# Optimization experiments

Hardware: AMD Instinct MI355X
Metric: run time of the kernel (lower is better)

The kernel has to match this reference:

```python
import jax, jax.numpy as jnp
from jax import lax
import numpy as np

B, C, H, W = 32, 256, 56, 56
K = 3
EPS = 1e-5


def setup_inputs() -> dict:
    key = jax.random.key(0)
    k1, k2, k3, k4 = jax.random.split(key, 4)
    x = jax.random.normal(k1, (B, C, H, W), dtype=jnp.float32)
    # xavier_normal init for conv weight [C_out, C_in, K, K]
    fan_in = C * K * K
    fan_out = C * K * K
    std = float(np.sqrt(2.0 / (fan_in + fan_out)))
    w = jax.random.normal(k2, (C, C, K, K), dtype=jnp.float32) * std
    gamma = jnp.ones((C,), dtype=jnp.float32)
    beta = jnp.zeros((C,), dtype=jnp.float32)
    return {"x": x, "w": w, "gamma": gamma, "beta": beta}


def reference(x, w, gamma, beta):
    # --- Binarize (bi_act_method=0, bi_w_scale=1) ---
    bx = jnp.sign(x)                                   # activation sign
    wc = jnp.clip(w, -1.0, 1.0)                        # fp_weight.data.clamp_(-1,1)
    mean_val = jnp.mean(jnp.abs(wc))
    bw = jnp.sign(wc) * mean_val                       # sign(w) * mean(|w|)
    # --- float conv2d, stride 1, padding 1 ---
    out = lax.conv_general_dilated(
        bx, bw, window_strides=(1, 1), padding=[(1, 1), (1, 1)],
        dimension_numbers=("NCHW", "OIHW", "NCHW"))
    # --- identity shortcut (stride=1, C_in==C_out) ---
    out = out + x
    # --- BatchNorm2d (training-mode batch stats, affine) ---
    mean = jnp.mean(out, axis=(0, 2, 3), keepdims=True)
    var = jnp.var(out, axis=(0, 2, 3), keepdims=True)
    out = (out - mean) * lax.rsqrt(var + EPS)
    out = out * gamma[None, :, None, None] + beta[None, :, None, None]
    # --- ReLU ---
    return jax.nn.relu(out)
```

## Files before the change

### kernel.cpp

```cpp
#include <hip/hip_runtime.h>
#include <cstdint>
#include <cstring>

#define Bn   32
#define Cn   256
#define Hn   56
#define Wn   56
#define HWn  (Hn*Wn)
#define NTOT (Bn*Cn*HWn)
#define WELEMS (Cn*Cn*9)
#define EPSv 1e-5f

#define F_WABS  0
#define F_SUM   64
#define F_SQ    320
#define F_SCALE 576
#define F_SHIFT 832
#define STATS_BYTES 4352
#define WB_OFF_BYTES  8192
#define XB_OFF_BYTES  131072

__global__ void pack_w_kernel(const float* __restrict__ w,
                              float* __restrict__ wsf,
                              uint32_t* __restrict__ wb) {
    int u = blockIdx.x * 256 + threadIdx.x;
    float sabs = 0.0f;
    {
        int co = u / 72;
        int r  = u % 72;
        int t  = r >> 3;
        int wd = r & 7;
        uint32_t bits = 0;
        const float* wp = w + (size_t)co * 2304 + (size_t)(wd * 32) * 9 + t;
        #pragma unroll
        for (int j = 0; j < 32; j++) {
            float wv = wp[(size_t)j * 9];
            sabs += fminf(fabsf(wv), 1.0f);
            bits |= (__float_as_uint(wv) >> 31) << j;
        }
        wb[u] = bits;
    }
    #pragma unroll
    for (int off = 32; off; off >>= 1) sabs += __shfl_down(sabs, off);
    __shared__ float sh[4];
    if ((threadIdx.x & 63) == 0) sh[threadIdx.x >> 6] = sabs;
    __syncthreads();
    if (threadIdx.x == 0)
        atomicAdd(&wsf[F_WABS], sh[0] + sh[1] + sh[2] + sh[3]);
}

__global__ void pack_x_kernel(const float* __restrict__ x,
                              uint32_t* __restrict__ xb) {
    int v = blockIdx.x * 256 + threadIdx.x;
    int b = v / HWn;
    int p = v % HWn;
    const float* xp = x + (size_t)b * Cn * HWn + p;
    uint32_t r[8];
    #pragma unroll
    for (int wd = 0; wd < 8; wd++) {
        uint32_t bits = 0;
        #pragma unroll
        for (int j = 0; j < 32; j++) {
            bits |= (__float_as_uint(xp[(size_t)(wd * 32 + j) * HWn]) >> 31) << j;
        }
        r[wd] = bits;
    }
    uint4* d = (uint4*)xb + (size_t)v * 2;
    d[0] = make_uint4(r[0], r[1], r[2], r[3]);
    d[1] = make_uint4(r[4], r[5], r[6], r[7]);
}

__global__ __launch_bounds__(256) void conv_kernel(
    const uint32_t* __restrict__ xb, const uint32_t* __restrict__ wb,
    const float* __restrict__ x, const float* __restrict__ wsf,
    float* __restrict__ out) {
    const int by  = blockIdx.x;
    const int cog = blockIdx.y;
    const int b   = blockIdx.z;
    const int tid = threadIdx.x;
    const int ty = tid >> 6, tx = tid & 63;
    const int y = by * 4 + ty;
    const bool active = tx < Wn;
    const int lx = tx < 55 ? tx : 55;

    const float mean_val = wsf[F_WABS] * (1.0f / (float)WELEMS);

    uint32_t nw[3][24];
    #pragma unroll
    for (int dh = 0; dh < 3; dh++) {
        int yy = y + dh - 1;
        int yc = yy < 0 ? 0 : (yy > 55 ? 55 : yy);
        const uint4* p = (const uint4*)xb + ((size_t)(b * HWn + yc * Wn + lx) * 2) - 2;
        uint4 q0 = p[0], q1 = p[1], q2 = p[2], q3 = p[3], q4 = p[4], q5 = p[5];
        nw[dh][0]=q0.x;  nw[dh][1]=q0.y;  nw[dh][2]=q0.z;  nw[dh][3]=q0.w;
        nw[dh][4]=q1.x;  nw[dh][5]=q1.y;  nw[dh][6]=q1.z;  nw[dh][7]=q1.w;
        nw[dh][8]=q2.x;  nw[dh][9]=q2.y;  nw[dh][10]=q2.z; nw[dh][11]=q2.w;
        nw[dh][12]=q3.x; nw[dh][13]=q3.y; nw[dh][14]=q3.z; nw[dh][15]=q3.w;
        nw[dh][16]=q4.x; nw[dh][17]=q4.y; nw[dh][18]=q4.z; nw[dh][19]=q4.w;
        nw[dh][20]=q5.x; nw[dh][21]=q5.y; nw[dh][22]=q5.z; nw[dh][23]=q5.w;
    }

    const int co0 = cog * 4;
    int pop[4] = {0, 0, 0, 0};
    int nv = 0;
    #pragma unroll
    for (int dh = 0; dh < 3; dh++) {
        bool rok = (unsigned)(y + dh - 1) < 56u;
        #pragma unroll
        for (int dw = 0; dw < 3; dw++) {
            bool ok = rok && ((unsigned)(tx + dw - 1) < 56u);
            if (ok) {
                nv++;
                #pragma unroll
                for (int cs = 0; cs < 4; cs++) {
                    const uint32_t* wp = wb + (size_t)(co0 + cs) * 72 + (dh * 3 + dw) * 8;
                    int pc = 0;
                    #pragma unroll
                    for (int wd = 0; wd < 8; wd++)
                        pc += __popc(nw[dh][dw * 8 + wd] ^ wp[wd]);
                    pop[cs] += pc;
                }
            }
        }
    }

    if (active) {
        #pragma unroll
        for (int cs = 0; cs < 4; cs++) {
            int c = co0 + cs;
            size_t idx = (size_t)(b * Cn + c) * HWn + y * Wn + tx;
            float dot = (float)(256 * nv - 2 * pop[cs]);
            out[idx] = mean_val * dot + x[idx];
        }
    }
}

__global__ void stats_kernel(const float* __restrict__ out,
                             float* __restrict__ wsf) {
    int plane = blockIdx.x;
    const float4* p = (const float4*)(out + (size_t)plane * HWn);
    float s = 0.0f, q = 0.0f;
    for (int i = threadIdx.x; i < HWn / 4; i += 256) {
        float4 v = p[i];
        s += v.x + v.y + v.z + v.w;
        q += v.x * v.x + v.y * v.y + v.z * v.z + v.w * v.w;
    }
    #pragma unroll
    for (int off = 32; off; off >>= 1) {
        s += __shfl_down(s, off);
        q += __shfl_down(q, off);
    }
    __shared__ float ss[4], sq[4];
    if ((threadIdx.x & 63) == 0) { ss[threadIdx.x >> 6] = s; sq[threadIdx.x >> 6] = q; }
    __syncthreads();
    if (threadIdx.x == 0) {
        int c = plane & 255;
        atomicAdd(&wsf[F_SUM + c], ss[0] + ss[1] + ss[2] + ss[3]);
        atomicAdd(&wsf[F_SQ  + c], sq[0] + sq[1] + sq[2] + sq[3]);
    }
}

__global__ void bnfinal_kernel(const float* __restrict__ g,
                               const float* __restrict__ bt,
                               float* __restrict__ wsf) {
    int c = threadIdx.x;
    const float n = (float)(Bn * HWn);
    float mean = wsf[F_SUM + c] / n;
    float var  = wsf[F_SQ + c] / n - mean * mean;
    float sc = g[c] * rsqrtf(var + EPSv);
    wsf[F_SCALE + c] = sc;
    wsf[F_SHIFT + c] = bt[c] - mean * sc;
}

__global__ void epilogue_kernel(float* __restrict__ out,
                                const float* __restrict__ wsf) {
    int i = blockIdx.x * 256 + threadIdx.x;
    float4* o4 = (float4*)out;
    float4 v = o4[i];
    int c = (i / (HWn / 4)) & 255;
    float sc = wsf[F_SCALE + c];
    float sh = wsf[F_SHIFT + c];
    v.x = fmaxf(v.x * sc + sh, 0.0f);
    v.y = fmaxf(v.y * sc + sh, 0.0f);
    v.z = fmaxf(v.z * sc + sh, 0.0f);
    v.w = fmaxf(v.w * sc + sh, 0.0f);
    o4[i] = v;
}

extern "C" void kernel_launch(void* const* d_in, const int* in_sizes, int n_in,
                              void* d_out, int out_size, void* d_ws, size_t ws_size,
                              hipStream_t stream) {
    const float* x     = (const float*)d_in[0];
    const float* w     = (const float*)d_in[1];
    const float* gamma = (const float*)d_in[2];
    const float* beta  = (const float*)d_in[3];
    float* out = (float*)d_out;

    float*    wsf = (float*)d_ws;
    uint32_t* wb  = (uint32_t*)((char*)d_ws + WB_OFF_BYTES);
    uint32_t* xb  = (uint32_t*)((char*)d_ws + XB_OFF_BYTES);

    hipMemsetAsync(d_ws, 0, STATS_BYTES, stream);
    pack_w_kernel<<<dim3(72), dim3(256), 0, stream>>>(w, wsf, wb);
    pack_x_kernel<<<dim3(392), dim3(256), 0, stream>>>(x, xb);
    conv_kernel<<<dim3(14, 64, 32), dim3(256), 0, stream>>>(xb, wb, x, wsf, out);
    stats_kernel<<<dim3(Bn * Cn), dim3(256), 0, stream>>>(out, wsf);
    bnfinal_kernel<<<dim3(1), dim3(256), 0, stream>>>(gamma, beta, wsf);
    epilogue_kernel<<<dim3(NTOT / 4 / 256), dim3(256), 0, stream>>>(out, wsf);
}
```

Measured before the change: 357.1 us.

## Use zero-padded bit-packed input with border correction table; widen output channels per thread

Packs sign bits into a zero-padded 58x58 layout so the conv inner loop has no boundary branches. Padding is corrected per output pixel with a precomputed per-channel table of weight popcount sums for each of nine border classes. Each thread now computes 8 output channels over a flat pixel index instead of 4, and the BN finalize step is folded into a per-plane epilogue. The cost is an extra memset of the padded buffer, an extra small kernel, and more registers per thread.

```diff
diff --git a/kernel.cpp b/kernel.cpp
--- a/kernel.cpp
+++ b/kernel.cpp
@@ -1,6 +1,5 @@
 #include <hip/hip_runtime.h>
 #include <cstdint>
-#include <cstring>
 
 #define Bn   32
 #define Cn   256
@@ -11,14 +10,17 @@
 #define WELEMS (Cn*Cn*9)
 #define EPSv 1e-5f
 
+#define PR   58
+#define PPB  (PR*PR)
+
 #define F_WABS  0
 #define F_SUM   64
 #define F_SQ    320
-#define F_SCALE 576
-#define F_SHIFT 832
-#define STATS_BYTES 4352
-#define WB_OFF_BYTES  8192
-#define XB_OFF_BYTES  131072
+#define STATS_BYTES 4096
+#define CLS_OFF_BYTES 4096
+#define WB_OFF_BYTES  16384
+#define XB_OFF_BYTES  98304
+#define XB_BYTES (Bn*PPB*8*4)
 
 __global__ void pack_w_kernel(const float* __restrict__ w,
                               float* __restrict__ wsf,
@@ -49,11 +51,40 @@
         atomicAdd(&wsf[F_WABS], sh[0] + sh[1] + sh[2] + sh[3]);
 }
 
+__global__ void wtable_kernel(const uint32_t* __restrict__ wb,
+                              int* __restrict__ clst) {
+    int co = threadIdx.x;
+    int wp[9];
+    #pragma unroll
+    for (int t = 0; t < 9; t++) {
+        int s = 0;
+        #pragma unroll
+        for (int wd = 0; wd < 8; wd++) s += __popc(wb[(co * 9 + t) * 8 + wd]);
+        wp[t] = 256 - 2 * s;
+    }
+    int T = wp[0] + wp[1] + wp[2];
+    int Bm = wp[6] + wp[7] + wp[8];
+    int L = wp[0] + wp[3] + wp[6];
+    int R = wp[2] + wp[5] + wp[8];
+    int* o = clst + co * 9;
+    o[0] = 0;
+    o[1] = L;
+    o[2] = R;
+    o[3] = T;
+    o[4] = T + L - wp[0];
+    o[5] = T + R - wp[2];
+    o[6] = Bm;
+    o[7] = Bm + L - wp[6];
+    o[8] = Bm + R - wp[8];
+}
+
 __global__ void pack_x_kernel(const float* __restrict__ x,
                               uint32_t* __restrict__ xb) {
     int v = blockIdx.x * 256 + threadIdx.x;
     int b = v / HWn;
-    int p = v % HWn;
+    int p = v - b * HWn;
+    int y = p / Wn;
+    int xq = p - y * Wn;
     const float* xp = x + (size_t)b * Cn * HWn + p;
     uint32_t r[8];
     #pragma unroll
@@ -65,73 +96,63 @@
         }
         r[wd] = bits;
     }
-    uint4* d = (uint4*)xb + (size_t)v * 2;
+    size_t dst = (size_t)b * PPB + (size_t)(y + 1) * PR + (xq + 1);
+    uint4* d = (uint4*)xb + dst * 2;
     d[0] = make_uint4(r[0], r[1], r[2], r[3]);
     d[1] = make_uint4(r[4], r[5], r[6], r[7]);
 }
 
 __global__ __launch_bounds__(256) void conv_kernel(
     const uint32_t* __restrict__ xb, const uint32_t* __restrict__ wb,
+    const int* __restrict__ clst,
     const float* __restrict__ x, const float* __restrict__ wsf,
     float* __restrict__ out) {
-    const int by  = blockIdx.x;
-    const int cog = blockIdx.y;
-    const int b   = blockIdx.z;
-    const int tid = threadIdx.x;
-    const int ty = tid >> 6, tx = tid & 63;
-    const int y = by * 4 + ty;
-    const bool active = tx < Wn;
-    const int lx = tx < 55 ? tx : 55;
+    int v = blockIdx.x * 256 + threadIdx.x;
+    int b = v / HWn;
+    int p = v - b * HWn;
+    int y = p / Wn;
+    int xq = p - y * Wn;
+    int co0 = blockIdx.y * 8;
 
     const float mean_val = wsf[F_WABS] * (1.0f / (float)WELEMS);
 
-    uint32_t nw[3][24];
+    const uint4* base = (const uint4*)xb + ((size_t)b * PPB + (size_t)y * PR + xq) * 2;
+
+    int acc[8] = {0, 0, 0, 0, 0, 0, 0, 0};
     #pragma unroll
     for (int dh = 0; dh < 3; dh++) {
-        int yy = y + dh - 1;
-        int yc = yy < 0 ? 0 : (yy > 55 ? 55 : yy);
-        const uint4* p = (const uint4*)xb + ((size_t)(b * HWn + yc * Wn + lx) * 2) - 2;
-        uint4 q0 = p[0], q1 = p[1], q2 = p[2], q3 = p[3], q4 = p[4], q5 = p[5];
-        nw[dh][0]=q0.x;  nw[dh][1]=q0.y;  nw[dh][2]=q0.z;  nw[dh][3]=q0.w;
-        nw[dh][4]=q1.x;  nw[dh][5]=q1.y;  nw[dh][6]=q1.z;  nw[dh][7]=q1.w;
-        nw[dh][8]=q2.x;  nw[dh][9]=q2.y;  nw[dh][10]=q2.z; nw[dh][11]=q2.w;
-        nw[dh][12]=q3.x; nw[dh][13]=q3.y; nw[dh][14]=q3.z; nw[dh][15]=q3.w;
-        nw[dh][16]=q4.x; nw[dh][17]=q4.y; nw[dh][18]=q4.z; nw[dh][19]=q4.w;
-        nw[dh][20]=q5.x; nw[dh][21]=q5.y; nw[dh][22]=q5.z; nw[dh][23]=q5.w;
-    }
-
-    const int co0 = cog * 4;
-    int pop[4] = {0, 0, 0, 0};
-    int nv = 0;
-    #pragma unroll
-    for (int dh = 0; dh < 3; dh++) {
-        bool rok = (unsigned)(y + dh - 1) < 56u;
+        uint32_t nw[24];
+        const uint4* rp = base + dh * (PR * 2);
+        #pragma unroll
+        for (int q = 0; q < 6; q++) {
+            uint4 t = rp[q];
+            nw[q * 4 + 0] = t.x; nw[q * 4 + 1] = t.y;
+            nw[q * 4 + 2] = t.z; nw[q * 4 + 3] = t.w;
+        }
         #pragma unroll
         for (int dw = 0; dw < 3; dw++) {
-            bool ok = rok && ((unsigned)(tx + dw - 1) < 56u);
-            if (ok) {
-                nv++;
+            #pragma unroll
+            for (int cs = 0; cs < 8; cs++) {
+                const uint32_t* wp = wb + ((size_t)(co0 + cs) * 9 + (dh * 3 + dw)) * 8;
+                int pc = acc[cs];
                 #pragma unroll
-                for (int cs = 0; cs < 4; cs++) {
-                    const uint32_t* wp = wb + (size_t)(co0 + cs) * 72 + (dh * 3 + dw) * 8;
-                    int pc = 0;
-                    #pragma unroll
-                    for (int wd = 0; wd < 8; wd++)
-                        pc += __popc(nw[dh][dw * 8 + wd] ^ wp[wd]);
-                    pop[cs] += pc;
-                }
+                for (int wd = 0; wd < 8; wd++)
+                    pc += __popc(nw[dw * 8 + wd] ^ wp[wd]);
+                acc[cs] = pc;
             }
         }
     }
 
-    if (active) {
-        #pragma unroll
-        for (int cs = 0; cs < 4; cs++) {
-            int c = co0 + cs;
-            size_t idx = (size_t)(b * Cn + c) * HWn + y * Wn + tx;
-            float dot = (float)(256 * nv - 2 * pop[cs]);
-            out[idx] = mean_val * dot + x[idx];
-        }
+    int yp = (y == 0) ? 1 : ((y == 55) ? 2 : 0);
+    int xp = (xq == 0) ? 1 : ((xq == 55) ? 2 : 0);
+    int cls = yp * 3 + xp;
+
+    #pragma unroll
+    for (int cs = 0; cs < 8; cs++) {
+        int corr = clst[(co0 + cs) * 9 + cls];
+        size_t idx = ((size_t)b * Cn + (co0 + cs)) * HWn + p;
+        float dot = (float)(2304 - 2 * acc[cs] - corr);
+        out[idx] = fmaf(mean_val, dot, x[idx]);
     }
 }
 
@@ -160,31 +181,26 @@
     }
 }
 
-__global__ void bnfinal_kernel(const float* __restrict__ g,
-                               const float* __restrict__ bt,
-                               float* __restrict__ wsf) {
-    int c = threadIdx.x;
+__global__ void epilogue_kernel(float* __restrict__ out,
+                                const float* __restrict__ wsf,
+                                const float* __restrict__ g,
+                                const float* __restrict__ bt) {
+    int plane = blockIdx.x;
+    int c = plane & 255;
     const float n = (float)(Bn * HWn);
     float mean = wsf[F_SUM + c] / n;
     float var  = wsf[F_SQ + c] / n - mean * mean;
     float sc = g[c] * rsqrtf(var + EPSv);
-    wsf[F_SCALE + c] = sc;
-    wsf[F_SHIFT + c] = bt[c] - mean * sc;
-}
-
-__global__ void epilogue_kernel(float* __restrict__ out,
-                                const float* __restrict__ wsf) {
-    int i = blockIdx.x * 256 + threadIdx.x;
-    float4* o4 = (float4*)out;
-    float4 v = o4[i];
-    int c = (i / (HWn / 4)) & 255;
-    float sc = wsf[F_SCALE + c];
-    float sh = wsf[F_SHIFT + c];
-    v.x = fmaxf(v.x * sc + sh, 0.0f);
-    v.y = fmaxf(v.y * sc + sh, 0.0f);
-    v.z = fmaxf(v.z * sc + sh, 0.0f);
-    v.w = fmaxf(v.w * sc + sh, 0.0f);
-    o4[i] = v;
+    float sh = bt[c] - mean * sc;
+    float4* o4 = (float4*)(out + (size_t)plane * HWn);
+    for (int i = threadIdx.x; i < HWn / 4; i += 256) {
+        float4 v = o4[i];
+        v.x = fmaxf(fmaf(v.x, sc, sh), 0.0f);
+        v.y = fmaxf(fmaf(v.y, sc, sh), 0.0f);
+        v.z = fmaxf(fmaf(v.z, sc, sh), 0.0f);
+        v.w = fmaxf(fmaf(v.w, sc, sh), 0.0f);
+        o4[i] = v;
+    }
 }
 
 extern "C" void kernel_launch(void* const* d_in, const int* in_sizes, int n_in,
@@ -196,15 +212,17 @@
     const float* beta  = (const float*)d_in[3];
     float* out = (float*)d_out;
 
-    float*    wsf = (float*)d_ws;
-    uint32_t* wb  = (uint32_t*)((char*)d_ws + WB_OFF_BYTES);
-    uint32_t* xb  = (uint32_t*)((char*)d_ws + XB_OFF_BYTES);
+    float*    wsf  = (float*)d_ws;
+    int*      clst = (int*)((char*)d_ws + CLS_OFF_BYTES);
+    uint32_t* wb   = (uint32_t*)((char*)d_ws + WB_OFF_BYTES);
+    uint32_t* xb   = (uint32_t*)((char*)d_ws + XB_OFF_BYTES);
 
     hipMemsetAsync(d_ws, 0, STATS_BYTES, stream);
+    hipMemsetAsync(xb, 0, XB_BYTES, stream);
     pack_w_kernel<<<dim3(72), dim3(256), 0, stream>>>(w, wsf, wb);
+    wtable_kernel<<<dim3(1), dim3(256), 0, stream>>>(wb, clst);
     pack_x_kernel<<<dim3(392), dim3(256), 0, stream>>>(x, xb);
-    conv_kernel<<<dim3(14, 64, 32), dim3(256), 0, stream>>>(xb, wb, x, wsf, out);
+    conv_kernel<<<dim3(392, 32), dim3(256), 0, stream>>>(xb, wb, clst, x, wsf, out);
     stats_kernel<<<dim3(Bn * Cn), dim3(256), 0, stream>>>(out, wsf);
-    bnfinal_kernel<<<dim3(1), dim3(256), 0, stream>>>(gamma, beta, wsf);
-    epilogue_kernel<<<dim3(NTOT / 4 / 256), dim3(256), 0, stream>>>(out, wsf);
-}
+    epilogue_kernel<<<dim3(Bn * Cn), dim3(256), 0, stream>>>(out, wsf, gamma, beta);
+}
```

After: 354.5 us. No clear change (-0.7%).
